# Optimization experiments

Hardware: AMD Instinct MI355X
Metric: run time of the kernel (lower is better)

Reference implementation:

```python
import jax, jax.numpy as jnp
import numpy as np

B, T, F, H = 64, 2048, 128, 32  # batch, seq_len, input_features, lstm hidden


def setup_inputs() -> dict:
    key = jax.random.key(0)
    ks = jax.random.split(key, 4)
    X = jax.random.normal(ks[0], (B, T, F), dtype=jnp.float32)
    # combined gate weights, order (i, f, g, o) as in flax.linen.LSTMCell
    Wx = jax.random.normal(ks[1], (F, 4 * H), dtype=jnp.float32) / np.float32(np.sqrt(F))
    Wh = jax.random.normal(ks[2], (H, 4 * H), dtype=jnp.float32) / np.float32(np.sqrt(H))
    b = jnp.zeros((4 * H,), dtype=jnp.float32)
    Wd = jax.random.normal(ks[3], (H, 1), dtype=jnp.float32) / np.float32(np.sqrt(H))
    bd = jnp.zeros((1,), dtype=jnp.float32)
    return {"X": X, "Wx": Wx, "Wh": Wh, "b": b, "Wd": Wd, "bd": bd}


def reference(X, Wx, Wh, b, Wd, bd):
    # Precompute input->gate projections for all timesteps in one GEMM.
    xg = jnp.einsum('btf,fg->btg', X, Wx) + b  # [B, T, 4H]

    def step(carry, xg_t):
        c, h = carry
        g = xg_t + h @ Wh  # [B, 4H]
        i, f, gc, o = jnp.split(g, 4, axis=-1)
        c = jax.nn.sigmoid(f) * c + jax.nn.sigmoid(i) * jnp.tanh(gc)
        h = jax.nn.sigmoid(o) * jnp.tanh(c)
        return (c, h), None

    zeros = jnp.zeros((X.shape[0], H), X.dtype)
    (c_T, h_T), _ = jax.lax.scan(step, (zeros, zeros), jnp.swapaxes(xg, 0, 1))
    # Dense(1) applied to outputs, then last timestep selected == Dense on h_T
    return h_T @ Wd + bd  # [B, 1]
```

## Files before the change

kernel.cpp:

```cpp
#include <hip/hip_runtime.h>
#include <math.h>

#define BB 64
#define TT 2048
#define FF 128
#define HH 32
#define GG 128

#define S1f (-1.4426950408889634f)
#define S2f (-2.8853900817779268f)

typedef _Float16 half2_t __attribute__((ext_vector_type(2)));

__device__ __forceinline__ unsigned h2u(half2_t v) {
    unsigned u; __builtin_memcpy(&u, &v, 4); return u;
}
__device__ __forceinline__ half2_t u2h(unsigned u) {
    half2_t v; __builtin_memcpy(&v, &u, 4); return v;
}
__device__ __forceinline__ half2_t pkrtz(float a, float b) {
    auto r = __builtin_amdgcn_cvt_pkrtz(a, b);
    half2_t v; __builtin_memcpy(&v, &r, 4); return v;
}
__device__ __forceinline__ float rcp_(float x) { return __builtin_amdgcn_rcpf(x); }
__device__ __forceinline__ float exp2_(float x) { return __builtin_amdgcn_exp2f(x); }

#define DPP_(x, ctrl) \
    ((unsigned)__builtin_amdgcn_mov_dpp((int)(x), (ctrl), 0xF, 0xF, true))
#define CTRL_XOR1 0xB1
#define CTRL_XOR2 0x4E
#define CTRL_ROR4 0x124
#define CTRL_ROR8 0x128
#define SWZ16_(x) ((unsigned)__builtin_amdgcn_ds_swizzle((int)(x), 0x401F))

#if __has_builtin(__builtin_amdgcn_permlane16_swap)
#define HAVE_PL16 1
#else
#define HAVE_PL16 0
#endif

__device__ __forceinline__ void gather_tree(unsigned v0, unsigned g[16]) {
    unsigned v1 = DPP_(v0, CTRL_XOR2);
#if HAVE_PL16
    auto sw = __builtin_amdgcn_permlane16_swap(v0, v1, false, false);
    unsigned s0 = (unsigned)sw[0], s1 = (unsigned)sw[1];
    g[0] = s0;
    g[1] = s1;
    g[2] = DPP_(s0, CTRL_XOR2);
    g[3] = DPP_(s1, CTRL_XOR2);
#else
    g[0] = v0;
    g[1] = v1;
    g[2] = SWZ16_(v0);
    g[3] = SWZ16_(v1);
#endif
#pragma unroll
    for (int r = 0; r < 4; ++r) g[4 + r] = DPP_(g[r], CTRL_ROR4);
#pragma unroll
    for (int r = 0; r < 8; ++r) g[8 + r] = DPP_(g[r], CTRL_ROR8);
}

__global__ __launch_bounds__(256) void xg_gemm(const float* __restrict__ X,
                                               const float* __restrict__ Wx,
                                               const float* __restrict__ bias,
                                               float* __restrict__ xgT) {
    __shared__ float XL[64 * 32];
    __shared__ float WL[32 * 128];
    const int tid = threadIdx.x;
    const int row0 = blockIdx.x * 64;
    const int j0 = (tid & 15) * 8;
    const int r0 = (tid >> 4) * 4;

    float acc[4][8];
#pragma unroll
    for (int r = 0; r < 4; ++r)
#pragma unroll
        for (int jj = 0; jj < 8; ++jj) acc[r][jj] = 0.f;

    for (int f0 = 0; f0 < FF; f0 += 32) {
        __syncthreads();
        {
            const float4* src = (const float4*)(Wx + f0 * GG);
            float4* dst = (float4*)WL;
            dst[tid]       = src[tid];
            dst[tid + 256] = src[tid + 256];
            dst[tid + 512] = src[tid + 512];
            dst[tid + 768] = src[tid + 768];
        }
        {
            int lin = tid * 4;
            int row = lin >> 5;
            int fi  = lin & 31;
            ((float4*)XL)[tid] =
                *(const float4*)(X + (size_t)(row0 + row) * FF + f0 + fi);
            lin = (tid + 256) * 4;
            row = lin >> 5;
            fi  = lin & 31;
            ((float4*)XL)[tid + 256] =
                *(const float4*)(X + (size_t)(row0 + row) * FF + f0 + fi);
        }
        __syncthreads();
#pragma unroll 4
        for (int fi = 0; fi < 32; ++fi) {
            float xv[4];
#pragma unroll
            for (int r = 0; r < 4; ++r) xv[r] = XL[(r0 + r) * 32 + fi];
            float4 w0 = *(float4*)&WL[fi * GG + j0];
            float4 w1 = *(float4*)&WL[fi * GG + j0 + 4];
            float w[8] = {w0.x, w0.y, w0.z, w0.w, w1.x, w1.y, w1.z, w1.w};
#pragma unroll
            for (int r = 0; r < 4; ++r)
#pragma unroll
                for (int jj = 0; jj < 8; ++jj)
                    acc[r][jj] = fmaf(xv[r], w[jj], acc[r][jj]);
        }
    }
    const int b  = row0 >> 11;
    const int t0 = (row0 & 2047) + r0;
    float bl[8];
#pragma unroll
    for (int jj = 0; jj < 8; ++jj) bl[jj] = bias[j0 + jj];
#pragma unroll
    for (int jj = 0; jj < 8; ++jj) {
        const int j = j0 + jj;
        const float sc = (j >= 64 && j < 96) ? S2f : S1f;
        float4 o;
        o.x = (acc[0][jj] + bl[jj]) * sc;
        o.y = (acc[1][jj] + bl[jj]) * sc;
        o.z = (acc[2][jj] + bl[jj]) * sc;
        o.w = (acc[3][jj] + bl[jj]) * sc;
        *(float4*)(xgT + ((size_t)b * GG + j) * TT + t0) = o;
    }
}

__global__ __launch_bounds__(64) void lstm_rec(const float* __restrict__ xgT,
                                               const float* __restrict__ Wh,
                                               const float* __restrict__ Wd,
                                               const float* __restrict__ bd,
                                               float* __restrict__ out) {
    const int l = threadIdx.x;
    const int m = l & 31;
    const bool lo = (l < HH);
    const int b = blockIdx.x;

    unsigned iv[16];
    gather_tree((unsigned)m, iv);

    const float scx = S1f;
    const float scy = lo ? S2f : S1f;
    half2_t whx[16], why[16];
#pragma unroll
    for (int r = 0; r < 16; ++r) {
        const int p  = (int)(iv[r] & 31u);
        const int p2 = p ^ 1;
        whx[r] = pkrtz(Wh[p * GG + l] * scx,       Wh[p2 * GG + l] * scx);
        why[r] = pkrtz(Wh[p * GG + l + 64] * scy,  Wh[p2 * GG + l + 64] * scy);
    }

    const float A1 = lo ? 2.f : 1.f;
    const float B1 = lo ? -1.f : 0.f;

    float h = 0.f;
    float c = 0.f;

    const float* pX = xgT + ((size_t)b * GG + l) * TT;
    const float* pY = xgT + ((size_t)b * GG + l + 64) * TT;

    float4 curX = *(const float4*)(pX);
    float4 curY = *(const float4*)(pY);
    float4 nxtX = *(const float4*)(pX + 4);
    float4 nxtY = *(const float4*)(pY + 4);

    auto step = [&](float xi, float xy) __attribute__((always_inline)) {
        unsigned hn = DPP_(__float_as_uint(h), CTRL_XOR1);
        unsigned g0 = h2u(pkrtz(h, __uint_as_float(hn)));
        unsigned g[16];
        gather_tree(g0, g);

        float ax[4] = {xi, 0.f, 0.f, 0.f};
        float ay[4] = {xy, 0.f, 0.f, 0.f};
#pragma unroll
        for (int r = 0; r < 16; ++r) {
            half2_t hp = u2h(g[r]);
            ax[r & 3] = __builtin_amdgcn_fdot2(hp, whx[r], ax[r & 3], false);
            ay[r & 3] = __builtin_amdgcn_fdot2(hp, why[r], ay[r & 3], false);
        }
        float a0 = (ax[0] + ax[1]) + (ax[2] + ax[3]);
        float a1 = (ay[0] + ay[1]) + (ay[2] + ay[3]);

        float act0 = rcp_(1.f + exp2_(a0));
        float act1 = fmaf(A1, rcp_(1.f + exp2_(a1)), B1);

        auto pq = __builtin_amdgcn_permlane32_swap(__float_as_uint(act0),
                                                   __float_as_uint(act1), false, false);
        auto uv = __builtin_amdgcn_permlane32_swap(__float_as_uint(act1),
                                                   __float_as_uint(act0), false, false);
        float p = __uint_as_float(pq[0]);
        float q = __uint_as_float(pq[1]);
        float u = __uint_as_float(uv[0]);
        float v = __uint_as_float(uv[1]);

        float f_all = lo ? q : act0;
        float o_all = lo ? v : act1;
        c = fmaf(f_all, c, u * p);
        float tc = fmaf(2.f, rcp_(1.f + exp2_(c * S2f)), -1.f);
        h = o_all * tc;
    };

#pragma unroll 1
    for (int t4 = 0; t4 < TT; t4 += 4) {
        float4 uX = curX, uY = curY;
        curX = nxtX; curY = nxtY;
        if (t4 + 8 < TT) {
            nxtX = *(const float4*)(pX + t4 + 8);
            nxtY = *(const float4*)(pY + t4 + 8);
        }
        step(uX.x, uY.x);
        step(uX.y, uY.y);
        step(uX.z, uY.z);
        step(uX.w, uY.w);
    }

    float contrib = h * Wd[m];
#pragma unroll
    for (int off = 32; off >= 1; off >>= 1)
        contrib += __shfl_xor(contrib, off, 64);
    if (l == 0) out[b] = fmaf(0.5f, contrib, bd[0]);
}

extern "C" void kernel_launch(void* const* d_in, const int* in_sizes, int n_in,
                              void* d_out, int out_size, void* d_ws, size_t ws_size,
                              hipStream_t stream) {
    const float* X    = (const float*)d_in[0];
    const float* Wx   = (const float*)d_in[1];
    const float* Wh   = (const float*)d_in[2];
    const float* bias = (const float*)d_in[3];
    const float* Wd   = (const float*)d_in[4];
    const float* bd   = (const float*)d_in[5];
    float* out = (float*)d_out;
    float* xgT = (float*)d_ws;

    hipLaunchKernelGGL(xg_gemm, dim3((BB * TT) / 64), dim3(256), 0, stream,
                       X, Wx, bias, xgT);
    hipLaunchKernelGGL(lstm_rec, dim3(BB), dim3(64), 0, stream,
                       xgT, Wh, Wd, bd, out);
}
```

Baseline: 500.2 us.

## Use fp16 fdot2 GEMM, pack gate projections as half2, simplify lane shuffles

The input-projection GEMM now converts X and Wx tiles to packed fp16 in shared memory and accumulates with fdot2. Its output is stored as packed half2 pairs (gate j and j+64) instead of fp32, which halves workspace traffic and gives one load stream per lane in the recurrence. The recurrence gather tree uses direct DPP row-rotate amounts instead of chained rotates, and the permlane32 swaps are simplified. Lower precision of the input projections and fp16 X may raise numerical error over 2048 steps.

New measurement: 454.5 us, median of 2. 9.1% less time.

```diff
diff --git a/kernel.cpp b/kernel.cpp
--- a/kernel.cpp
+++ b/kernel.cpp
@@ -24,13 +24,14 @@
 }
 __device__ __forceinline__ float rcp_(float x) { return __builtin_amdgcn_rcpf(x); }
 __device__ __forceinline__ float exp2_(float x) { return __builtin_amdgcn_exp2f(x); }
+__device__ __forceinline__ float fdot2_(half2_t a, half2_t b, float c) {
+    return __builtin_amdgcn_fdot2(a, b, c, false);
+}
 
 #define DPP_(x, ctrl) \
     ((unsigned)__builtin_amdgcn_mov_dpp((int)(x), (ctrl), 0xF, 0xF, true))
 #define CTRL_XOR1 0xB1
 #define CTRL_XOR2 0x4E
-#define CTRL_ROR4 0x124
-#define CTRL_ROR8 0x128
 #define SWZ16_(x) ((unsigned)__builtin_amdgcn_ds_swizzle((int)(x), 0x401F))
 
 #if __has_builtin(__builtin_amdgcn_permlane16_swap)
@@ -40,35 +41,33 @@
 #endif
 
 __device__ __forceinline__ void gather_tree(unsigned v0, unsigned g[16]) {
+#if HAVE_PL16
     unsigned v1 = DPP_(v0, CTRL_XOR2);
-#if HAVE_PL16
     auto sw = __builtin_amdgcn_permlane16_swap(v0, v1, false, false);
     unsigned s0 = (unsigned)sw[0], s1 = (unsigned)sw[1];
-    g[0] = s0;
-    g[1] = s1;
-    g[2] = DPP_(s0, CTRL_XOR2);
-    g[3] = DPP_(s1, CTRL_XOR2);
 #else
-    g[0] = v0;
-    g[1] = v1;
-    g[2] = SWZ16_(v0);
-    g[3] = SWZ16_(v1);
+    unsigned s0 = v0;
+    unsigned s1 = SWZ16_(v0);
 #endif
-#pragma unroll
-    for (int r = 0; r < 4; ++r) g[4 + r] = DPP_(g[r], CTRL_ROR4);
-#pragma unroll
-    for (int r = 0; r < 8; ++r) g[8 + r] = DPP_(g[r], CTRL_ROR8);
+    g[0] = s0;                 g[1] = s1;
+    g[2]  = DPP_(s0, 0x122);   g[3]  = DPP_(s1, 0x122);
+    g[4]  = DPP_(s0, 0x124);   g[5]  = DPP_(s1, 0x124);
+    g[6]  = DPP_(s0, 0x126);   g[7]  = DPP_(s1, 0x126);
+    g[8]  = DPP_(s0, 0x128);   g[9]  = DPP_(s1, 0x128);
+    g[10] = DPP_(s0, 0x12A);   g[11] = DPP_(s1, 0x12A);
+    g[12] = DPP_(s0, 0x12C);   g[13] = DPP_(s1, 0x12C);
+    g[14] = DPP_(s0, 0x12E);   g[15] = DPP_(s1, 0x12E);
 }
 
 __global__ __launch_bounds__(256) void xg_gemm(const float* __restrict__ X,
                                                const float* __restrict__ Wx,
                                                const float* __restrict__ bias,
-                                               float* __restrict__ xgT) {
-    __shared__ float XL[64 * 32];
-    __shared__ float WL[32 * 128];
+                                               unsigned* __restrict__ xg2) {
+    __shared__ unsigned XLh[64][16];
+    __shared__ unsigned WLh[16][128];
     const int tid = threadIdx.x;
     const int row0 = blockIdx.x * 64;
-    const int j0 = (tid & 15) * 8;
+    const int j0 = (tid & 15) * 4;
     const int r0 = (tid >> 4) * 4;
 
     float acc[4][8];
@@ -80,60 +79,64 @@
     for (int f0 = 0; f0 < FF; f0 += 32) {
         __syncthreads();
         {
-            const float4* src = (const float4*)(Wx + f0 * GG);
-            float4* dst = (float4*)WL;
-            dst[tid]       = src[tid];
-            dst[tid + 256] = src[tid + 256];
-            dst[tid + 512] = src[tid + 512];
-            dst[tid + 768] = src[tid + 768];
+            const int jq = (tid & 31) * 4;
+#pragma unroll
+            for (int qq = 0; qq < 2; ++qq) {
+                const int q = (tid >> 5) + qq * 8;
+                float4 wa = *(const float4*)(Wx + (size_t)(f0 + 2 * q) * GG + jq);
+                float4 wb = *(const float4*)(Wx + (size_t)(f0 + 2 * q + 1) * GG + jq);
+                WLh[q][jq + 0] = h2u(pkrtz(wa.x, wb.x));
+                WLh[q][jq + 1] = h2u(pkrtz(wa.y, wb.y));
+                WLh[q][jq + 2] = h2u(pkrtz(wa.z, wb.z));
+                WLh[q][jq + 3] = h2u(pkrtz(wa.w, wb.w));
+            }
         }
         {
             int lin = tid * 4;
-            int row = lin >> 5;
-            int fi  = lin & 31;
-            ((float4*)XL)[tid] =
-                *(const float4*)(X + (size_t)(row0 + row) * FF + f0 + fi);
+            int row = lin >> 5, fi = lin & 31;
+            float4 x = *(const float4*)(X + (size_t)(row0 + row) * FF + f0 + fi);
+            XLh[row][(fi >> 1) + 0] = h2u(pkrtz(x.x, x.y));
+            XLh[row][(fi >> 1) + 1] = h2u(pkrtz(x.z, x.w));
             lin = (tid + 256) * 4;
-            row = lin >> 5;
-            fi  = lin & 31;
-            ((float4*)XL)[tid + 256] =
-                *(const float4*)(X + (size_t)(row0 + row) * FF + f0 + fi);
+            row = lin >> 5; fi = lin & 31;
+            x = *(const float4*)(X + (size_t)(row0 + row) * FF + f0 + fi);
+            XLh[row][(fi >> 1) + 0] = h2u(pkrtz(x.x, x.y));
+            XLh[row][(fi >> 1) + 1] = h2u(pkrtz(x.z, x.w));
         }
         __syncthreads();
 #pragma unroll 4
-        for (int fi = 0; fi < 32; ++fi) {
-            float xv[4];
-#pragma unroll
-            for (int r = 0; r < 4; ++r) xv[r] = XL[(r0 + r) * 32 + fi];
-            float4 w0 = *(float4*)&WL[fi * GG + j0];
-            float4 w1 = *(float4*)&WL[fi * GG + j0 + 4];
-            float w[8] = {w0.x, w0.y, w0.z, w0.w, w1.x, w1.y, w1.z, w1.w};
+        for (int q = 0; q < 16; ++q) {
+            half2_t xv[4];
+#pragma unroll
+            for (int r = 0; r < 4; ++r) xv[r] = u2h(XLh[r0 + r][q]);
+            uint4 w0 = *(uint4*)&WLh[q][j0];
+            uint4 w1 = *(uint4*)&WLh[q][j0 + 64];
+            unsigned wj[8] = {w0.x, w0.y, w0.z, w0.w, w1.x, w1.y, w1.z, w1.w};
 #pragma unroll
             for (int r = 0; r < 4; ++r)
 #pragma unroll
                 for (int jj = 0; jj < 8; ++jj)
-                    acc[r][jj] = fmaf(xv[r], w[jj], acc[r][jj]);
+                    acc[r][jj] = fdot2_(xv[r], u2h(wj[jj]), acc[r][jj]);
         }
     }
     const int b  = row0 >> 11;
     const int t0 = (row0 & 2047) + r0;
-    float bl[8];
-#pragma unroll
-    for (int jj = 0; jj < 8; ++jj) bl[jj] = bias[j0 + jj];
-#pragma unroll
-    for (int jj = 0; jj < 8; ++jj) {
+#pragma unroll
+    for (int jj = 0; jj < 4; ++jj) {
         const int j = j0 + jj;
-        const float sc = (j >= 64 && j < 96) ? S2f : S1f;
-        float4 o;
-        o.x = (acc[0][jj] + bl[jj]) * sc;
-        o.y = (acc[1][jj] + bl[jj]) * sc;
-        o.z = (acc[2][jj] + bl[jj]) * sc;
-        o.w = (acc[3][jj] + bl[jj]) * sc;
-        *(float4*)(xgT + ((size_t)b * GG + j) * TT + t0) = o;
-    }
-}
-
-__global__ __launch_bounds__(64) void lstm_rec(const float* __restrict__ xgT,
+        const float bX = bias[j];
+        const float bY = bias[j + 64];
+        const float sY = (j < 32) ? S2f : S1f;
+        uint4 o;
+        o.x = h2u(pkrtz((acc[0][jj] + bX) * S1f, (acc[0][jj + 4] + bY) * sY));
+        o.y = h2u(pkrtz((acc[1][jj] + bX) * S1f, (acc[1][jj + 4] + bY) * sY));
+        o.z = h2u(pkrtz((acc[2][jj] + bX) * S1f, (acc[2][jj + 4] + bY) * sY));
+        o.w = h2u(pkrtz((acc[3][jj] + bX) * S1f, (acc[3][jj + 4] + bY) * sY));
+        *(uint4*)(xg2 + (size_t)(b * 64 + j) * TT + t0) = o;
+    }
+}
+
+__global__ __launch_bounds__(64) void lstm_rec(const unsigned* __restrict__ xg2,
                                                const float* __restrict__ Wh,
                                                const float* __restrict__ Wd,
                                                const float* __restrict__ bd,
@@ -163,62 +166,53 @@
     float h = 0.f;
     float c = 0.f;
 
-    const float* pX = xgT + ((size_t)b * GG + l) * TT;
-    const float* pY = xgT + ((size_t)b * GG + l + 64) * TT;
-
-    float4 curX = *(const float4*)(pX);
-    float4 curY = *(const float4*)(pY);
-    float4 nxtX = *(const float4*)(pX + 4);
-    float4 nxtY = *(const float4*)(pY + 4);
-
-    auto step = [&](float xi, float xy) __attribute__((always_inline)) {
+    const unsigned* pX = xg2 + (size_t)(b * 64 + l) * TT;
+
+    uint4 cur = *(const uint4*)(pX);
+    uint4 nxt = *(const uint4*)(pX + 4);
+
+    auto step = [&](unsigned w) __attribute__((always_inline)) {
+        half2_t xv = u2h(w);
+        float xi = (float)xv[0];
+        float xy = (float)xv[1];
         unsigned hn = DPP_(__float_as_uint(h), CTRL_XOR1);
         unsigned g0 = h2u(pkrtz(h, __uint_as_float(hn)));
         unsigned g[16];
         gather_tree(g0, g);
-
         float ax[4] = {xi, 0.f, 0.f, 0.f};
         float ay[4] = {xy, 0.f, 0.f, 0.f};
 #pragma unroll
         for (int r = 0; r < 16; ++r) {
             half2_t hp = u2h(g[r]);
-            ax[r & 3] = __builtin_amdgcn_fdot2(hp, whx[r], ax[r & 3], false);
-            ay[r & 3] = __builtin_amdgcn_fdot2(hp, why[r], ay[r & 3], false);
+            ax[r & 3] = fdot2_(hp, whx[r], ax[r & 3]);
+            ay[r & 3] = fdot2_(hp, why[r], ay[r & 3]);
         }
         float a0 = (ax[0] + ax[1]) + (ax[2] + ax[3]);
         float a1 = (ay[0] + ay[1]) + (ay[2] + ay[3]);
-
         float act0 = rcp_(1.f + exp2_(a0));
         float act1 = fmaf(A1, rcp_(1.f + exp2_(a1)), B1);
-
-        auto pq = __builtin_amdgcn_permlane32_swap(__float_as_uint(act0),
-                                                   __float_as_uint(act1), false, false);
-        auto uv = __builtin_amdgcn_permlane32_swap(__float_as_uint(act1),
-                                                   __float_as_uint(act0), false, false);
-        float p = __uint_as_float(pq[0]);
-        float q = __uint_as_float(pq[1]);
-        float u = __uint_as_float(uv[0]);
-        float v = __uint_as_float(uv[1]);
-
-        float f_all = lo ? q : act0;
-        float o_all = lo ? v : act1;
-        c = fmaf(f_all, c, u * p);
+        auto sw0 = __builtin_amdgcn_permlane32_swap(__float_as_uint(act0),
+                                                    __float_as_uint(act0), false, false);
+        auto sw1 = __builtin_amdgcn_permlane32_swap(__float_as_uint(act1),
+                                                    __float_as_uint(act1), false, false);
+        float i_all = __uint_as_float(sw0[0]);
+        float f_all = __uint_as_float(sw0[1]);
+        float g_all = __uint_as_float(sw1[0]);
+        float o_all = __uint_as_float(sw1[1]);
+        c = fmaf(f_all, c, i_all * g_all);
         float tc = fmaf(2.f, rcp_(1.f + exp2_(c * S2f)), -1.f);
         h = o_all * tc;
     };
 
 #pragma unroll 1
     for (int t4 = 0; t4 < TT; t4 += 4) {
-        float4 uX = curX, uY = curY;
-        curX = nxtX; curY = nxtY;
-        if (t4 + 8 < TT) {
-            nxtX = *(const float4*)(pX + t4 + 8);
-            nxtY = *(const float4*)(pY + t4 + 8);
-        }
-        step(uX.x, uY.x);
-        step(uX.y, uY.y);
-        step(uX.z, uY.z);
-        step(uX.w, uY.w);
+        uint4 u = cur;
+        cur = nxt;
+        if (t4 + 8 < TT) nxt = *(const uint4*)(pX + t4 + 8);
+        step(u.x);
+        step(u.y);
+        step(u.z);
+        step(u.w);
     }
 
     float contrib = h * Wd[m];
@@ -238,10 +232,10 @@
     const float* Wd   = (const float*)d_in[4];
     const float* bd   = (const float*)d_in[5];
     float* out = (float*)d_out;
-    float* xgT = (float*)d_ws;
+    unsigned* xg2 = (unsigned*)d_ws;
 
     hipLaunchKernelGGL(xg_gemm, dim3((BB * TT) / 64), dim3(256), 0, stream,
-                       X, Wx, bias, xgT);
+                       X, Wx, bias, xg2);
     hipLaunchKernelGGL(lstm_rec, dim3(BB), dim3(64), 0, stream,
-                       xgT, Wh, Wd, bd, out);
-}
+                       xg2, Wh, Wd, bd, out);
+}
```
